# Kernel tuning notes

Hardware: AMD Instinct MI355X
Metric: run time of the kernel (lower is better)

The kernel has to match this reference:

```python
import jax, jax.numpy as jnp
import numpy as np
import math

EPS = 0.1
N_ITER = 200
SCALE = 1.0
ATOL = 1e-4
RTOL = 1e-4
THRESH = 100.0
D = 2
LOGZ = math.log((2.0 * math.pi * EPS) ** (D / 2.0))


def setup_inputs() -> dict:
    key = jax.random.key(0)
    k1, k2 = jax.random.split(key)
    n, m = 4096, 4096
    # points scaled so C/eps stays O(1) -> K well within fp32 range
    x_spt = 0.3 * jax.random.normal(k1, (n, D), dtype=jnp.float32)
    y_spt = 0.3 * jax.random.normal(k2, (m, D), dtype=jnp.float32)
    x_w = jnp.ones((n,), jnp.float32) / n
    y_w = jnp.ones((m,), jnp.float32) / m
    return {"x_w": x_w, "x_spt": x_spt, "y_w": y_w, "y_spt": y_spt}


def _cdist2(x, y):
    # squared euclidean distance matrix [n, m] via gemm form
    x2 = jnp.sum(x * x, axis=1)
    y2 = jnp.sum(y * y, axis=1)
    d2 = x2[:, None] + y2[None, :] - 2.0 * (x @ y.T)
    return jnp.maximum(d2, 0.0)


def _getK(C, x_w, y_w, a, b):
    return jnp.exp(-(C + a[:, None] + b[None, :]) / EPS - LOGZ) * x_w[:, None] * y_w[None, :]


def _sinkhorn(C, x_w, y_w):
    # balanced Sinkhorn fixed point with absorption/stabilization, mirrors torch loop
    n, m = C.shape
    u0 = jnp.ones((n,), C.dtype)
    v0 = jnp.ones((m,), C.dtype)
    a0 = jnp.zeros((n,), C.dtype)
    b0 = jnp.zeros((m,), C.dtype)
    K0 = _getK(C, x_w, y_w, a0, b0)
    yw_norm = jnp.max(jnp.abs(y_w))

    def cond(st):
        i, u, v, a, b, K, done = st
        return (i < N_ITER) & (~done)

    def body(st):
        i, u, v, a, b, K, done = st
        v = y_w / (K.T @ u)      # proxdiv_balanced
        u = x_w / (K @ v)
        err = jnp.max(jnp.abs(v * (K.T @ u) - y_w))
        done = (err < ATOL) | (err / yw_norm < RTOL)
        stab = (jnp.maximum(jnp.max(jnp.abs(u)), jnp.max(jnp.abs(v))) > THRESH) & (~done)

        def do_stab(ops):
            u_, v_, a_, b_, K_ = ops
            a2 = a_ - EPS * jnp.log(u_)
            b2 = b_ - EPS * jnp.log(v_)
            return (jnp.ones_like(u_), jnp.ones_like(v_), a2, b2, _getK(C, x_w, y_w, a2, b2))

        u, v, a, b, K = jax.lax.cond(stab, do_stab, lambda ops: ops, (u, v, a, b, K))
        return (i + 1, u, v, a, b, K, done)

    st = jax.lax.while_loop(cond, body, (jnp.int32(0), u0, v0, a0, b0, K0, jnp.bool_(False)))
    return st[1], st[2], st[3], st[4]


def _obj_dual(C, x_w, y_w, u, v, a, b):
    f = -EPS * jnp.log(u) + a
    g = -EPS * jnp.log(v) + b
    f_cts = EPS * jax.nn.logsumexp((-C - g[None, :]) / EPS + jnp.log(y_w)[None, :], axis=1) - EPS * LOGZ
    g_cts = EPS * jax.nn.logsumexp((-C - f[:, None]) / EPS + jnp.log(x_w)[:, None], axis=0) - EPS * LOGZ
    f1 = f_cts @ x_w   # F_indicator_star (balanced)
    f2 = g_cts @ y_w
    plan = jnp.exp(-(C + f_cts[:, None] + g_cts[None, :]) / EPS - LOGZ) * x_w[:, None] * y_w[None, :]
    return -f1 - f2 - EPS * jnp.sum(plan)


def reference(x_w, x_spt, y_w, y_spt):
    C = _cdist2(x_spt, y_spt) / (2.0 * SCALE ** 2)
    u, v, a, b = _sinkhorn(C, x_w, y_w)
    return _obj_dual(C, x_w, y_w, u, v, a, b)
```

## Files before the change

kernel.cpp:

```cpp
#include <hip/hip_runtime.h>
#include <math.h>

#define N 4096

static constexpr float F_EPS     = 0.1f;
static constexpr float F_EPSLOGZ = -0.046470802658470075f;
static constexpr float F_ATOL    = 1e-4f;
static constexpr float F_RTOL    = 1e-4f;
static constexpr int   NITER     = 200;
static constexpr int   NB        = 256;
static constexpr int   BT        = 256;
static constexpr float K2        = 14.426950408889634f;
static constexpr float HK2       = 7.213475204444817f;
static constexpr float C1        = -0.6704311637146724f;
static constexpr float LN2       = 0.6931471805599453f;

__device__ __forceinline__ float wsum(float x) {
#pragma unroll
  for (int o = 32; o; o >>= 1) x += __shfl_xor(x, o, 64);
  return x;
}
__device__ __forceinline__ float wmax(float x) {
#pragma unroll
  for (int o = 32; o; o >>= 1) x = fmaxf(x, __shfl_xor(x, o, 64));
  return x;
}

__device__ __forceinline__ float aload(const float* p) {
  return __hip_atomic_load(p, __ATOMIC_RELAXED, __HIP_MEMORY_SCOPE_AGENT);
}
__device__ __forceinline__ void astore(float* p, float v) {
  __hip_atomic_store(p, v, __ATOMIC_RELAXED, __HIP_MEMORY_SCOPE_AGENT);
}
__device__ __forceinline__ unsigned uload(const unsigned* p) {
  return __hip_atomic_load(p, __ATOMIC_RELAXED, __HIP_MEMORY_SCOPE_AGENT);
}

__device__ __forceinline__ void gbar(unsigned* sync, int bid, unsigned tgt) {
  asm volatile("s_waitcnt vmcnt(0)" ::: "memory");
  __syncthreads();
  if (threadIdx.x == 0) {
    unsigned* leaf = sync + ((bid & 15) << 4);
    unsigned* root = sync + 256;
    unsigned* flag = sync + 272 + ((bid & 15) << 4);
    const unsigned old = __hip_atomic_fetch_add(leaf, 1u, __ATOMIC_RELAXED, __HIP_MEMORY_SCOPE_AGENT);
    if ((old & 15u) == 15u) {
      const unsigned r = __hip_atomic_fetch_add(root, 1u, __ATOMIC_RELAXED, __HIP_MEMORY_SCOPE_AGENT);
      if ((r & 15u) == 15u) {
#pragma unroll
        for (int q = 0; q < 16; ++q)
          __hip_atomic_store(sync + 272 + (q << 4), tgt, __ATOMIC_RELAXED, __HIP_MEMORY_SCOPE_AGENT);
      }
    }
    while (uload(flag) < tgt) __builtin_amdgcn_s_sleep(2);
  }
  __syncthreads();
}

__global__ void zero_kernel(unsigned* sync) {
  const int t = threadIdx.x;
  if (t < 544) __hip_atomic_store(&sync[t], 0u, __ATOMIC_RELAXED, __HIP_MEMORY_SCOPE_AGENT);
}

__global__ void __launch_bounds__(BT) fused_kernel(
    const float* __restrict__ xw, const float2* __restrict__ xs,
    const float* __restrict__ yw, const float2* __restrict__ ys,
    float* __restrict__ pcol, float* __restrict__ prow, float* __restrict__ psav,
    float* __restrict__ berr, float* __restrict__ fcg, float* __restrict__ gcg,
    float* __restrict__ part, float* __restrict__ out, unsigned* __restrict__ sync) {
  __shared__ __align__(16) float2 xk[N];
  __shared__ __align__(16) float2 yk[N];
  __shared__ __align__(16) float  P[N];
  __shared__ float ew[4];
  const int tid  = threadIdx.x, bid = blockIdx.x;
  const int lane = tid & 63,    wib = tid >> 6;
  const int c0   = bid * 16 + wib * 4;
  unsigned tgt = 0;

  float mv = 0.f;
  for (int k = tid; k < N; k += BT) {
    const float2 xp = xs[k];
    const float2 yp = ys[k];
    xk[k] = make_float2(K2 * xp.x, K2 * xp.y);
    yk[k] = make_float2(K2 * yp.x, K2 * yp.y);
    P[k]  = log2f(xw[k]) - HK2 * (xp.x * xp.x + xp.y * xp.y);
    mv = fmaxf(mv, fabsf(yw[k]));
  }
  mv = wmax(mv);
  if (lane == 0) ew[wib] = mv;
  __syncthreads();
  const float ywn = fmaxf(fmaxf(ew[0], ew[1]), fmaxf(ew[2], ew[3]));
  __syncthreads();

  float2 xr[4], yc[4];
  float l2xw[4], l2yw[4], ywc[4];
#pragma unroll
  for (int q = 0; q < 4; ++q) {
    xr[q] = xs[c0 + q];
    yc[q] = ys[c0 + q];
    l2xw[q] = log2f(xw[c0 + q]);
    l2yw[q] = log2f(yw[c0 + q]);
    ywc[q]  = yw[c0 + q];
  }

  float accPrev[4];
  {
    float a[4] = {0.f, 0.f, 0.f, 0.f};
#pragma unroll 8
    for (int t = 0; t < 64; ++t) {
      const int i = (t << 6) + lane;
      const float2 c = xk[i]; const float w = P[i];
#pragma unroll
      for (int q = 0; q < 4; ++q)
        a[q] += exp2f(fmaf(c.x, yc[q].x, fmaf(c.y, yc[q].y, w)));
    }
#pragma unroll
    for (int q = 0; q < 4; ++q) {
      a[q] = wsum(a[q]);
      accPrev[q] = a[q];
      if (lane == 0) astore(&prow[c0 + q], l2yw[q] - log2f(a[q]));
    }
  }
  tgt++; gbar(sync, bid, tgt);

  int converged = 0;
  for (int it = 0; it < NITER && !converged; ++it) {
    {
      float tmp[16];
#pragma unroll
      for (int q = 0; q < 16; ++q) tmp[q] = aload(&prow[tid + (q << 8)]);
#pragma unroll
      for (int q = 0; q < 16; ++q) P[tid + (q << 8)] = tmp[q];
    }
    __syncthreads();
    if (tid < 16) astore(&psav[(bid << 4) + tid], P[(bid << 4) + tid]);
    {
      float a[4] = {0.f, 0.f, 0.f, 0.f};
#pragma unroll 8
      for (int t = 0; t < 64; ++t) {
        const int j = (t << 6) + lane;
        const float2 c = yk[j]; const float w = P[j];
#pragma unroll
        for (int q = 0; q < 4; ++q)
          a[q] += exp2f(fmaf(c.x, xr[q].x, fmaf(c.y, xr[q].y, w)));
      }
#pragma unroll
      for (int q = 0; q < 4; ++q) {
        a[q] = wsum(a[q]);
        if (lane == 0) astore(&pcol[c0 + q], l2xw[q] - log2f(a[q]));
      }
    }
    tgt++; gbar(sync, bid, tgt);

    {
      float tmp[16];
#pragma unroll
      for (int q = 0; q < 16; ++q) tmp[q] = aload(&pcol[tid + (q << 8)]);
#pragma unroll
      for (int q = 0; q < 16; ++q) P[tid + (q << 8)] = tmp[q];
    }
    __syncthreads();
    {
      float a[4] = {0.f, 0.f, 0.f, 0.f};
#pragma unroll 8
      for (int t = 0; t < 64; ++t) {
        const int i = (t << 6) + lane;
        const float2 c = xk[i]; const float w = P[i];
#pragma unroll
        for (int q = 0; q < 4; ++q)
          a[q] += exp2f(fmaf(c.x, yc[q].x, fmaf(c.y, yc[q].y, w)));
      }
      float e = 0.f;
#pragma unroll
      for (int q = 0; q < 4; ++q) {
        a[q] = wsum(a[q]);
        e = fmaxf(e, ywc[q] * fabsf(a[q] / accPrev[q] - 1.0f));
        accPrev[q] = a[q];
        if (lane == 0) astore(&prow[c0 + q], l2yw[q] - log2f(a[q]));
      }
      if (lane == 0) ew[wib] = e;
    }
    __syncthreads();
    if (tid == 0) astore(&berr[bid], fmaxf(fmaxf(ew[0], ew[1]), fmaxf(ew[2], ew[3])));
    tgt++; gbar(sync, bid, tgt);

    float m = wmax(aload(&berr[tid]));
    if (lane == 0) ew[wib] = m;
    __syncthreads();
    const float err = fmaxf(fmaxf(ew[0], ew[1]), fmaxf(ew[2], ew[3]));
    __syncthreads();
    if ((err < F_ATOL) || (err / ywn < F_RTOL)) converged = 1;
  }

  {
    const int half = bid >> 7;
    const int base = (bid & 127) * 32 + wib * 8;
    {
      float tmp[16];
      if (half == 0) {
#pragma unroll
        for (int q = 0; q < 16; ++q) tmp[q] = aload(&psav[tid + (q << 8)]) + C1;
      } else {
#pragma unroll
        for (int q = 0; q < 16; ++q) tmp[q] = aload(&pcol[tid + (q << 8)]);
      }
#pragma unroll
      for (int q = 0; q < 16; ++q) P[tid + (q << 8)] = tmp[q];
    }
    __syncthreads();
    float2 rc[8]; float sq2[8]; float acc[8];
#pragma unroll
    for (int q = 0; q < 8; ++q) {
      const int r = base + q;
      rc[q] = half ? ys[r] : xs[r];
      sq2[q] = rc[q].x * rc[q].x + rc[q].y * rc[q].y;
      acc[q] = 0.f;
    }
    if (half == 0) {
#pragma unroll 4
      for (int t = 0; t < 64; ++t) {
        const int j = (t << 6) + lane;
        const float2 c = yk[j]; const float w = P[j];
#pragma unroll
        for (int q = 0; q < 8; ++q)
          acc[q] += exp2f(fmaf(c.x, rc[q].x, fmaf(c.y, rc[q].y, w)));
      }
    } else {
#pragma unroll 4
      for (int t = 0; t < 64; ++t) {
        const int i = (t << 6) + lane;
        const float2 c = xk[i]; const float w = P[i];
#pragma unroll
        for (int q = 0; q < 8; ++q)
          acc[q] += exp2f(fmaf(c.x, rc[q].x, fmaf(c.y, rc[q].y, w)));
      }
    }
#pragma unroll
    for (int q = 0; q < 8; ++q) acc[q] = wsum(acc[q]);
    if (lane == 0) {
#pragma unroll
      for (int q = 0; q < 8; ++q) {
        const int r = base + q;
        const float val = F_EPS * fmaf(LN2, log2f(acc[q]), -5.f * sq2[q]) - F_EPSLOGZ;
        astore(half ? &gcg[r] : &fcg[r], val);
      }
    }
  }
  tgt++; gbar(sync, bid, tgt);

  {
    {
      float tmp[16];
#pragma unroll
      for (int q = 0; q < 16; ++q) tmp[q] = aload(&gcg[tid + (q << 8)]);
#pragma unroll
      for (int q = 0; q < 16; ++q) {
        const int k = tid + (q << 8);
        const float2 yp = ys[k];
        const float y2k = yp.x * yp.x + yp.y * yp.y;
        P[k] = fmaf(-HK2, y2k, fmaf(-K2, tmp[q], log2f(yw[k]))) - C1;
      }
    }
    __syncthreads();
    float a[4], wx[4];
#pragma unroll
    for (int q = 0; q < 4; ++q) {
      const int r = c0 + q;
      const float x2r = xr[q].x * xr[q].x + xr[q].y * xr[q].y;
      wx[q] = fmaf(-HK2, x2r, fmaf(-K2, aload(&fcg[r]), l2xw[q]));
      a[q] = 0.f;
    }
#pragma unroll 8
    for (int t = 0; t < 64; ++t) {
      const int j = (t << 6) + lane;
      const float2 c = yk[j]; const float w = P[j];
#pragma unroll
      for (int q = 0; q < 4; ++q)
        a[q] += exp2f(fmaf(c.x, xr[q].x, fmaf(c.y, xr[q].y, w)));
    }
#pragma unroll
    for (int q = 0; q < 4; ++q) a[q] = wsum(a[q]);
    if (lane == 0)
      ew[wib] = ((exp2f(wx[0]) * a[0] + exp2f(wx[1]) * a[1]) +
                 (exp2f(wx[2]) * a[2] + exp2f(wx[3]) * a[3]));
    __syncthreads();
    if (tid == 0) astore(&part[bid], (ew[0] + ew[1]) + (ew[2] + ew[3]));
  }
  tgt++; gbar(sync, bid, tgt);

  if (bid == 0) {
    float a1 = 0.f, a2 = 0.f;
    for (int i = tid; i < N; i += BT) {
      a1 += aload(&fcg[i]) * xw[i];
      a2 += aload(&gcg[i]) * yw[i];
    }
    const float a3 = aload(&part[tid]);
    float* r1 = P; float* r2 = P + 256; float* r3 = P + 512;
    r1[tid] = a1; r2[tid] = a2; r3[tid] = a3; __syncthreads();
    for (int s2 = 128; s2; s2 >>= 1) {
      if (tid < s2) { r1[tid] += r1[tid + s2]; r2[tid] += r2[tid + s2]; r3[tid] += r3[tid + s2]; }
      __syncthreads();
    }
    if (tid == 0) out[0] = -r1[0] - r2[0] - F_EPS * r3[0];
  }
}

extern "C" void kernel_launch(void* const* d_in, const int* in_sizes, int n_in,
                              void* d_out, int out_size, void* d_ws, size_t ws_size,
                              hipStream_t stream) {
  const float*  xw  = (const float*)d_in[0];
  const float2* xs2 = (const float2*)d_in[1];
  const float*  yw  = (const float*)d_in[2];
  const float2* ys2 = (const float2*)d_in[3];
  float* out = (float*)d_out;

  float* w = (float*)d_ws;
  float *pcol = w,          *prow = w + 4096,  *psav = w + 8192,
        *fcg  = w + 12288,  *gcg  = w + 16384,
        *berr = w + 20480,  *part = w + 20736;
  unsigned* sync = (unsigned*)(w + 20992);

  zero_kernel<<<1, 576, 0, stream>>>(sync);
  fused_kernel<<<NB, BT, 0, stream>>>(xw, xs2, yw, ys2,
                                      pcol, prow, psav, berr, fcg, gcg, part, out, sync);
}
```

Before: 144.5 us.

## Replace tree grid barrier with block-0 polled flags and fold convergence test

```diff
diff --git a/kernel.cpp b/kernel.cpp
--- a/kernel.cpp
+++ b/kernel.cpp
@@ -14,6 +14,7 @@
 static constexpr float HK2       = 7.213475204444817f;
 static constexpr float C1        = -0.6704311637146724f;
 static constexpr float LN2       = 0.6931471805599453f;
+static constexpr unsigned SALT   = 0x40000000u;
 
 __device__ __forceinline__ float wsum(float x) {
 #pragma unroll
@@ -35,31 +36,39 @@
 __device__ __forceinline__ unsigned uload(const unsigned* p) {
   return __hip_atomic_load(p, __ATOMIC_RELAXED, __HIP_MEMORY_SCOPE_AGENT);
 }
-
-__device__ __forceinline__ void gbar(unsigned* sync, int bid, unsigned tgt) {
+__device__ __forceinline__ void ustore(unsigned* p, unsigned v) {
+  __hip_atomic_store(p, v, __ATOMIC_RELAXED, __HIP_MEMORY_SCOPE_AGENT);
+}
+
+__device__ __forceinline__ int gbar(unsigned* __restrict__ sync, const float* __restrict__ berr,
+                                    float* __restrict__ sred, int* __restrict__ sdone,
+                                    int bid, int tid, int lane, int wib,
+                                    unsigned tgt, int decide, float ywn) {
   asm volatile("s_waitcnt vmcnt(0)" ::: "memory");
   __syncthreads();
-  if (threadIdx.x == 0) {
-    unsigned* leaf = sync + ((bid & 15) << 4);
-    unsigned* root = sync + 256;
-    unsigned* flag = sync + 272 + ((bid & 15) << 4);
-    const unsigned old = __hip_atomic_fetch_add(leaf, 1u, __ATOMIC_RELAXED, __HIP_MEMORY_SCOPE_AGENT);
-    if ((old & 15u) == 15u) {
-      const unsigned r = __hip_atomic_fetch_add(root, 1u, __ATOMIC_RELAXED, __HIP_MEMORY_SCOPE_AGENT);
-      if ((r & 15u) == 15u) {
-#pragma unroll
-        for (int q = 0; q < 16; ++q)
-          __hip_atomic_store(sync + 272 + (q << 4), tgt, __ATOMIC_RELAXED, __HIP_MEMORY_SCOPE_AGENT);
-      }
-    }
-    while (uload(flag) < tgt) __builtin_amdgcn_s_sleep(2);
+  if (tid == 0) ustore(&sync[bid << 2], SALT + tgt);
+  if (bid == 0) {
+    while (uload(&sync[tid << 2]) != SALT + tgt) __builtin_amdgcn_s_sleep(1);
+    __syncthreads();
+    unsigned rel = SALT + (tgt << 1);
+    if (decide) {
+      const float m = wmax(aload(&berr[tid]));
+      if (lane == 0) sred[wib] = m;
+      __syncthreads();
+      const float err = fmaxf(fmaxf(sred[0], sred[1]), fmaxf(sred[2], sred[3]));
+      if ((err < F_ATOL) || (err / ywn < F_RTOL)) rel |= 1u;
+      __syncthreads();
+    }
+    if (tid < 16) ustore(&sync[1024 + (tid << 4)], rel);
+  }
+  if (tid == 0) {
+    unsigned f;
+    unsigned* flag = &sync[1024 + ((bid & 15) << 4)];
+    while (((f = uload(flag)) & ~1u) != SALT + (tgt << 1)) __builtin_amdgcn_s_sleep(1);
+    *sdone = (int)(f & 1u);
   }
   __syncthreads();
-}
-
-__global__ void zero_kernel(unsigned* sync) {
-  const int t = threadIdx.x;
-  if (t < 544) __hip_atomic_store(&sync[t], 0u, __ATOMIC_RELAXED, __HIP_MEMORY_SCOPE_AGENT);
+  return *sdone;
 }
 
 __global__ void __launch_bounds__(BT) fused_kernel(
@@ -72,6 +81,8 @@
   __shared__ __align__(16) float2 yk[N];
   __shared__ __align__(16) float  P[N];
   __shared__ float ew[4];
+  __shared__ float sred[4];
+  __shared__ int   sdone;
   const int tid  = threadIdx.x, bid = blockIdx.x;
   const int lane = tid & 63,    wib = tid >> 6;
   const int c0   = bid * 16 + wib * 4;
@@ -121,7 +132,7 @@
       if (lane == 0) astore(&prow[c0 + q], l2yw[q] - log2f(a[q]));
     }
   }
-  tgt++; gbar(sync, bid, tgt);
+  tgt++; gbar(sync, berr, sred, &sdone, bid, tid, lane, wib, tgt, 0, ywn);
 
   int converged = 0;
   for (int it = 0; it < NITER && !converged; ++it) {
@@ -150,7 +161,7 @@
         if (lane == 0) astore(&pcol[c0 + q], l2xw[q] - log2f(a[q]));
       }
     }
-    tgt++; gbar(sync, bid, tgt);
+    tgt++; gbar(sync, berr, sred, &sdone, bid, tid, lane, wib, tgt, 0, ywn);
 
     {
       float tmp[16];
@@ -182,14 +193,8 @@
     }
     __syncthreads();
     if (tid == 0) astore(&berr[bid], fmaxf(fmaxf(ew[0], ew[1]), fmaxf(ew[2], ew[3])));
-    tgt++; gbar(sync, bid, tgt);
-
-    float m = wmax(aload(&berr[tid]));
-    if (lane == 0) ew[wib] = m;
-    __syncthreads();
-    const float err = fmaxf(fmaxf(ew[0], ew[1]), fmaxf(ew[2], ew[3]));
-    __syncthreads();
-    if ((err < F_ATOL) || (err / ywn < F_RTOL)) converged = 1;
+    tgt++;
+    converged = gbar(sync, berr, sred, &sdone, bid, tid, lane, wib, tgt, 1, ywn);
   }
 
   {
@@ -246,7 +251,7 @@
       }
     }
   }
-  tgt++; gbar(sync, bid, tgt);
+  tgt++; gbar(sync, berr, sred, &sdone, bid, tid, lane, wib, tgt, 0, ywn);
 
   {
     {
@@ -286,7 +291,7 @@
     __syncthreads();
     if (tid == 0) astore(&part[bid], (ew[0] + ew[1]) + (ew[2] + ew[3]));
   }
-  tgt++; gbar(sync, bid, tgt);
+  tgt++; gbar(sync, berr, sred, &sdone, bid, tid, lane, wib, tgt, 0, ywn);
 
   if (bid == 0) {
     float a1 = 0.f, a2 = 0.f;
@@ -320,7 +325,6 @@
         *berr = w + 20480,  *part = w + 20736;
   unsigned* sync = (unsigned*)(w + 20992);
 
-  zero_kernel<<<1, 576, 0, stream>>>(sync);
   fused_kernel<<<NB, BT, 0, stream>>>(xw, xs2, yw, ys2,
                                       pcol, prow, psav, berr, fcg, gcg, part, out, sync);
 }
```

Result: faster. 139.5 us (-3.5%).
